# Performance work log

Measured on AMD Instinct MI355X. Metric: run time of the kernel, lower is better.

## Reference

```python
import jax, jax.numpy as jnp
import numpy as np

EPS = 1e-5  # torch BatchNorm1d default

def setup_inputs() -> dict:
    B, I, O, F = 32, 512, 720, 321
    key = jax.random.key(0)
    k = jax.random.split(key, 7)
    x = jax.random.normal(k[0], (B, I, F), dtype=jnp.float32)
    # per-timestep Linear weights stacked: W[f] is the f-th nn.Linear (out, in)
    bound = 1.0 / np.sqrt(I)
    W = jax.random.uniform(k[1], (F, O, I), dtype=jnp.float32, minval=-bound, maxval=bound)
    b = jax.random.uniform(k[2], (F, O), dtype=jnp.float32, minval=-bound, maxval=bound)
    # BatchNorm1d(num_feats) affine params + running stats (eval-mode semantics)
    gamma = jnp.ones((F,), dtype=jnp.float32)
    beta = jnp.zeros((F,), dtype=jnp.float32)
    running_mean = jax.random.normal(k[3], (F,), dtype=jnp.float32) * 0.1
    running_var = jax.random.uniform(k[4], (F,), dtype=jnp.float32, minval=0.5, maxval=1.5)
    return {"x": x, "W": W, "b": b, "gamma": gamma, "beta": beta,
            "running_mean": running_mean, "running_var": running_var}

def reference(x, W, b, gamma, beta, running_mean, running_var):
    # x: [B, I, F]. BatchNorm1d over the feature (F) channel, applied elementwise
    # over batch and in_channels (permute/permute in torch is just a broadcast here).
    inv = gamma * jax.lax.rsqrt(running_var + EPS)          # [F]
    xn = x * inv + (beta - running_mean * inv)              # [B, I, F]
    # 321 independent Linears fused into one batched GEMM:
    # out[b, o, f] = sum_i xn[b, i, f] * W[f, o, i] + b[f, o]
    out = jnp.einsum('bif,foi->bof', xn, W) + b.T[None]     # [B, O, F]
    return out
```

## Files before the change

### kernel.cpp

```cpp
#include <hip/hip_runtime.h>
#include <stdint.h>

#define F_DIM 321
#define O_DIM 720
#define I_DIM 512
#define B_DIM 32
#define G_F 8

typedef __attribute__((ext_vector_type(8))) short short8;
typedef __attribute__((ext_vector_type(4))) float f32x4;
typedef __attribute__((ext_vector_type(4))) uint32_t u32x4;

__device__ __forceinline__ uint32_t rne_pack2(float lo, float hi) {
  uint32_t a = __builtin_bit_cast(uint32_t, lo);
  uint32_t b = __builtin_bit_cast(uint32_t, hi);
  a += 0x7FFFu + ((a >> 16) & 1u);
  b += 0x7FFFu + ((b >> 16) & 1u);
  return (a >> 16) | (b & 0xFFFF0000u);
}

__global__ void __launch_bounds__(256) xn_pack_kernel(
    const float* __restrict__ x, const float* __restrict__ gamma,
    const float* __restrict__ beta, const float* __restrict__ rmean,
    const float* __restrict__ rvar, u32x4* __restrict__ ws) {
  __shared__ float tile[8 * F_DIM];
  const int iblk = blockIdx.x;
  const int b    = blockIdx.y;
  const float* src = x + ((size_t)b * I_DIM + (size_t)iblk * 8) * F_DIM;
  for (int idx = threadIdx.x; idx < 8 * F_DIM; idx += 256)
    tile[idx] = src[idx];
  __syncthreads();
  for (int f = threadIdx.x; f < F_DIM; f += 256) {
    float inv = gamma[f] * rsqrtf(rvar[f] + 1e-5f);
    float sh  = beta[f] - rmean[f] * inv;
    float v[8];
#pragma unroll
    for (int j = 0; j < 8; ++j) v[j] = fmaf(tile[j * F_DIM + f], inv, sh);
    u32x4 pk;
    pk.x = rne_pack2(v[0], v[1]);
    pk.y = rne_pack2(v[2], v[3]);
    pk.z = rne_pack2(v[4], v[5]);
    pk.w = rne_pack2(v[6], v[7]);
    ws[(size_t)f * 2048 + iblk * 32 + b] = pk;
  }
}

__global__ void __launch_bounds__(256) linear_bn_kernel(
    const float* __restrict__ Wt, const float* __restrict__ bias,
    const u32x4* __restrict__ xn, float* __restrict__ out) {
  __shared__ u32x4 lds[2048];
  const int tid  = threadIdx.x;
  const int lane = tid & 63;
  const int wv   = tid >> 6;
  const int quad = lane >> 4;
  const int t16  = lane & 15;
  const int mtile = wv & 1;
  const int ntile = wv >> 1;
  const int kkh   = wv >> 1;
  const int ntS   = wv & 1;
  const int o0 = blockIdx.x * 32;
  const int fb = blockIdx.y * G_F;
  const int nf = min(G_F, F_DIM - fb);
  const int sRow  = ntS * 16 + (lane >> 2);
  const int sQuad = lane & 3;
  const int oS = min(o0 + sRow, O_DIM - 1);
  const int oC = o0 + ntile * 16 + t16;

  f32x4 acc[G_F];
#pragma unroll
  for (int ff = 0; ff < G_F; ++ff) {
    float bv = 0.0f;
    if (ff < nf && oC < O_DIM) bv = bias[(size_t)(fb + ff) * O_DIM + oC];
    acc[ff] = (f32x4){bv, bv, bv, bv};
  }

  u32x4 pk[8];
  auto stage_load = [&](int f) {
    const float* base =
        Wt + ((size_t)f * O_DIM + oS) * I_DIM + kkh * 256 + sQuad * 8;
#pragma unroll
    for (int j = 0; j < 8; ++j) {
      f32x4 a = *(const f32x4*)(base + j * 32);
      f32x4 b = *(const f32x4*)(base + j * 32 + 4);
      u32x4 p;
      p.x = rne_pack2(a.x, a.y);
      p.y = rne_pack2(a.z, a.w);
      p.z = rne_pack2(b.x, b.y);
      p.w = rne_pack2(b.z, b.w);
      pk[j] = p;
    }
  };

  stage_load(fb);
#pragma unroll
  for (int ff = 0; ff < G_F; ++ff) {
    if (ff >= nf) break;
    __syncthreads();
#pragma unroll
    for (int j = 0; j < 8; ++j)
      lds[(kkh * 8 + j) * 128 + ntS * 64 + lane] = pk[j];
    __syncthreads();
    if (ff + 1 < nf) stage_load(fb + ff + 1);
    const int f = fb + ff;
    const u32x4* xf = xn + (size_t)f * 2048 + mtile * 16 + t16;
#pragma unroll
    for (int kk = 0; kk < 16; ++kk) {
      u32x4 av = xf[(kk * 4 + quad) * 32];
      u32x4 bv = lds[kk * 128 + ntile * 64 + (t16 << 2) + quad];
      acc[ff] = __builtin_amdgcn_mfma_f32_16x16x32_bf16(
          __builtin_bit_cast(short8, av), __builtin_bit_cast(short8, bv),
          acc[ff], 0, 0, 0);
    }
  }

  if (oC < O_DIM) {
#pragma unroll
    for (int r = 0; r < 4; ++r) {
      const int brow = mtile * 16 + quad * 4 + r;
      float* po = out + ((size_t)brow * O_DIM + oC) * F_DIM + fb;
#pragma unroll
      for (int ff = 0; ff < G_F; ++ff)
        if (ff < nf) po[ff] = acc[ff][r];
    }
  }
}

extern "C" void kernel_launch(void* const* d_in, const int* in_sizes, int n_in,
                              void* d_out, int out_size, void* d_ws, size_t ws_size,
                              hipStream_t stream) {
  const float* x     = (const float*)d_in[0];
  const float* W     = (const float*)d_in[1];
  const float* b     = (const float*)d_in[2];
  const float* gamma = (const float*)d_in[3];
  const float* beta  = (const float*)d_in[4];
  const float* rmean = (const float*)d_in[5];
  const float* rvar  = (const float*)d_in[6];
  u32x4* ws = (u32x4*)d_ws;

  xn_pack_kernel<<<dim3(64, 32), 256, 0, stream>>>(x, gamma, beta, rmean, rvar, ws);
  linear_bn_kernel<<<dim3(23, 41), 256, 0, stream>>>(W, b, ws, (float*)d_out);
}
```

Baseline: 743.1 us.

## Coalesce W row loads, swizzle LDS layout, and remap blocks across XCDs

The W staging now has 128 threads read contiguous 16-byte chunks along each full 512-element row, two rows per step, instead of 32-byte pieces scattered across rows. Packed bf16 pairs are written to LDS in a row-major layout with an XOR swizzle so the 16-byte MFMA operand reads avoid bank conflicts. Block IDs are also remapped so consecutive tiles land on the same XCD, which should improve L2 reuse of x-normalized data and W. The trade-off is more, smaller 8-byte LDS stores and extra index arithmetic.

```diff
diff --git a/kernel.cpp b/kernel.cpp
--- a/kernel.cpp
+++ b/kernel.cpp
@@ -10,6 +10,7 @@
 typedef __attribute__((ext_vector_type(8))) short short8;
 typedef __attribute__((ext_vector_type(4))) float f32x4;
 typedef __attribute__((ext_vector_type(4))) uint32_t u32x4;
+typedef __attribute__((ext_vector_type(2))) uint32_t u32x2;
 
 __device__ __forceinline__ uint32_t rne_pack2(float lo, float hi) {
   uint32_t a = __builtin_bit_cast(uint32_t, lo);
@@ -48,7 +49,8 @@
 __global__ void __launch_bounds__(256) linear_bn_kernel(
     const float* __restrict__ Wt, const float* __restrict__ bias,
     const u32x4* __restrict__ xn, float* __restrict__ out) {
-  __shared__ u32x4 lds[2048];
+  __shared__ u32x4 lds4[2048];
+  char* ldsb = (char*)lds4;
   const int tid  = threadIdx.x;
   const int lane = tid & 63;
   const int wv   = tid >> 6;
@@ -56,15 +58,20 @@
   const int t16  = lane & 15;
   const int mtile = wv & 1;
   const int ntile = wv >> 1;
-  const int kkh   = wv >> 1;
-  const int ntS   = wv & 1;
-  const int o0 = blockIdx.x * 32;
-  const int fb = blockIdx.y * G_F;
+
+  const int d   = blockIdx.y * 23 + blockIdx.x;
+  const int xcd = d & 7, idx = d >> 3;
+  const int w   = (xcd < 7) ? xcd * 118 + idx : 826 + idx;
+  const int bx  = w % 23;
+  const int by  = w / 23;
+
+  const int o0 = bx * 32;
+  const int fb = by * G_F;
   const int nf = min(G_F, F_DIM - fb);
-  const int sRow  = ntS * 16 + (lane >> 2);
-  const int sQuad = lane & 3;
-  const int oS = min(o0 + sRow, O_DIM - 1);
   const int oC = o0 + ntile * 16 + t16;
+
+  const int sc  = tid & 127;
+  const int shi = tid >> 7;
 
   f32x4 acc[G_F];
 #pragma unroll
@@ -74,19 +81,16 @@
     acc[ff] = (f32x4){bv, bv, bv, bv};
   }
 
-  u32x4 pk[8];
+  u32x2 pk[16];
   auto stage_load = [&](int f) {
-    const float* base =
-        Wt + ((size_t)f * O_DIM + oS) * I_DIM + kkh * 256 + sQuad * 8;
+    const float* fbase = Wt + (size_t)f * (O_DIM * I_DIM) + sc * 4;
 #pragma unroll
-    for (int j = 0; j < 8; ++j) {
-      f32x4 a = *(const f32x4*)(base + j * 32);
-      f32x4 b = *(const f32x4*)(base + j * 32 + 4);
-      u32x4 p;
+    for (int j = 0; j < 16; ++j) {
+      const int row = min(o0 + 2 * j + shi, O_DIM - 1);
+      f32x4 a = *(const f32x4*)(fbase + (size_t)row * I_DIM);
+      u32x2 p;
       p.x = rne_pack2(a.x, a.y);
       p.y = rne_pack2(a.z, a.w);
-      p.z = rne_pack2(b.x, b.y);
-      p.w = rne_pack2(b.z, b.w);
       pk[j] = p;
     }
   };
@@ -97,16 +101,22 @@
     if (ff >= nf) break;
     __syncthreads();
 #pragma unroll
-    for (int j = 0; j < 8; ++j)
-      lds[(kkh * 8 + j) * 128 + ntS * 64 + lane] = pk[j];
+    for (int j = 0; j < 16; ++j) {
+      const int o = 2 * j + shi;
+      const int byte = ((o * 128 + sc) * 8) ^ ((o & 7) << 4);
+      *(u32x2*)(ldsb + byte) = pk[j];
+    }
     __syncthreads();
     if (ff + 1 < nf) stage_load(fb + ff + 1);
     const int f = fb + ff;
     const u32x4* xf = xn + (size_t)f * 2048 + mtile * 16 + t16;
+    const int orow = ntile * 16 + t16;
+    const int swz  = (t16 & 7) << 4;
 #pragma unroll
     for (int kk = 0; kk < 16; ++kk) {
       u32x4 av = xf[(kk * 4 + quad) * 32];
-      u32x4 bv = lds[kk * 128 + ntile * 64 + (t16 << 2) + quad];
+      u32x4 bv = *(const u32x4*)(
+          ldsb + ((orow * 1024 + kk * 64 + quad * 16) ^ swz));
       acc[ff] = __builtin_amdgcn_mfma_f32_16x16x32_bf16(
           __builtin_bit_cast(short8, av), __builtin_bit_cast(short8, bv),
           acc[ff], 0, 0, 0);
```

New measurement: 679.3 us. 1.09x faster.
